# Optimization experiments

Hardware: AMD Instinct MI355X
Metric: run time of the kernel (lower is better)

## Reference

```python
import jax, jax.numpy as jnp
import numpy as np

N_NODES = 100000
N_EDGES = 800000
DIM = 128
BN_EPS = 1e-5


def setup_inputs() -> dict:
    key = jax.random.key(0)
    k1, k2, k3 = jax.random.split(key, 3)
    x = jax.random.normal(k1, (N_NODES, DIM), dtype=jnp.float32)
    edge_index = jax.random.randint(k2, (2, N_EDGES), 0, N_NODES, dtype=jnp.int64)
    # xavier-uniform-like init for the linear weight [out, in]
    limit = float(np.sqrt(6.0 / (DIM + DIM)))
    W = jax.random.uniform(k3, (DIM, DIM), dtype=jnp.float32, minval=-limit, maxval=limit)
    bias = jnp.zeros((DIM,), dtype=jnp.float32)
    bn_gamma = jnp.ones((DIM,), dtype=jnp.float32)
    bn_beta = jnp.zeros((DIM,), dtype=jnp.float32)
    return {"x": x, "edge_index": edge_index, "W": W, "bias": bias,
            "bn_gamma": bn_gamma, "bn_beta": bn_beta, "bit_sum": 0}


def reference(x, edge_index, W, bias, bn_gamma, bn_beta, bit_sum):
    n = x.shape[0]
    # Linear (no bias), is_q=False path; q_xw treated as identity.
    h = x @ W.T                                   # [N, D]
    row, col = edge_index[0], edge_index[1]
    # symmetric degree normalization: deg computed over destination (col)
    deg = jax.ops.segment_sum(jnp.ones_like(col, dtype=h.dtype), col, num_segments=n)
    deg_inv_sqrt = jnp.where(deg > 0, jax.lax.rsqrt(jnp.maximum(deg, 1.0)), 0.0)
    norm = deg_inv_sqrt[row] * deg_inv_sqrt[col]  # [E]
    # message: norm * x_j (x_j = h[row]), aggregate (add) at col
    msg = norm[:, None] * h[row]                  # [E, D]
    out = jax.ops.segment_sum(msg, col, num_segments=n)  # [N, D]
    out = out + bias
    # BatchNorm1d (training mode: batch stats, biased variance)
    mean = jnp.mean(out, axis=0)
    var = jnp.var(out, axis=0)
    out = (out - mean) * jax.lax.rsqrt(var + BN_EPS) * bn_gamma + bn_beta
    # activation
    out = jax.nn.relu(out)
    # residual (in_dim == out_dim); dropout p=0 -> identity
    out = out + x
    return (out, 0)
```

## Files before the change

### kernel.cpp

```cpp
#include <hip/hip_runtime.h>
#include <cstddef>

#define NN 100000
#define DD 128
#define ND (NN * DD)
#define BN_EPS 1e-5f
#define LDA 136
#define NREP 16
#define NBKT 98
#define EPB 4096

typedef __bf16 bf16_t;
typedef bf16_t bf16x8 __attribute__((ext_vector_type(8)));
typedef float f32x4 __attribute__((ext_vector_type(4)));
typedef unsigned int uint;
typedef unsigned short ushort;


__device__ __forceinline__ ushort f2b(float f) {
    uint u = __builtin_bit_cast(uint, f);
    u += 0x7FFFu + ((u >> 16) & 1u);
    return (ushort)(u >> 16);
}
__device__ __forceinline__ float b2f(uint s) {
    return __builtin_bit_cast(float, s << 16);
}

__device__ __forceinline__ int detect_i64(const int* __restrict__ ei) {
    __shared__ int sflag;
    int t = threadIdx.x;
    if (t < 64) {
        int hi = ei[2 * t + 1];
        unsigned long long b = __ballot(hi == 0);
        if (t == 0) sflag = (b == ~0ull) ? 1 : 0;
    }
    __syncthreads();
    return sflag;
}

__global__ __launch_bounds__(256) void k_prep(const int* __restrict__ ei,
                                              int* __restrict__ bktot, int E, int nbh,
                                              const float* __restrict__ x,
                                              uint* __restrict__ xb,
                                              const float* __restrict__ W,
                                              uint* __restrict__ wb) {
    if ((int)blockIdx.x < nbh) {
        int f = detect_i64(ei);
        __shared__ int hist[NBKT];
        int t = threadIdx.x;
        if (t < NBKT) hist[t] = 0;
        __syncthreads();
        int base = blockIdx.x * EPB;
        int count = min(EPB, E - base);
        for (int i = t; i < count; i += 256) {
            int e = base + i;
            int c = f ? ei[2 * (E + e)] : ei[E + e];
            atomicAdd(&hist[c >> 10], 1);
        }
        __syncthreads();
        if (t < NBKT && hist[t] > 0) atomicAdd(&bktot[t], hist[t]);
        return;
    }
    int i = (blockIdx.x - nbh) * 256 + threadIdx.x;
    const float* src;
    uint* dst;
    int j;
    if (i < ND / 8) { src = x; dst = xb; j = i; }
    else { j = i - ND / 8; if (j >= (DD * DD) / 8) return; src = W; dst = wb; }
    const float4* s4 = (const float4*)src;
    float4 a = s4[2 * j], b = s4[2 * j + 1];
    uint4 o;
    o.x = (uint)f2b(a.x) | ((uint)f2b(a.y) << 16);
    o.y = (uint)f2b(a.z) | ((uint)f2b(a.w) << 16);
    o.z = (uint)f2b(b.x) | ((uint)f2b(b.y) << 16);
    o.w = (uint)f2b(b.z) | ((uint)f2b(b.w) << 16);
    ((uint4*)dst)[j] = o;
}

__global__ __launch_bounds__(256) void k_bin(const int* __restrict__ ei,
                                             const int* __restrict__ bktot,
                                             int* __restrict__ bcur,
                                             uint2* __restrict__ pairs, int E) {
    int f = detect_i64(ei);
    __shared__ int bb[NBKT], hist[NBKT], scur[NBKT];
    int t = threadIdx.x;
    if (t < NBKT) { bb[t] = bktot[t]; hist[t] = 0; }
    __syncthreads();
    if (t == 0) {
        int run = 0;
        for (int i = 0; i < NBKT; ++i) { int v = bb[i]; bb[i] = run; run += v; }
    }
    int base = blockIdx.x * EPB;
    int count = min(EPB, E - base);
    int rr[16], cc[16];
#pragma unroll
    for (int k = 0; k < 16; ++k) {
        int i = t + k * 256;
        if (i < count) {
            int e = base + i;
            int r, c;
            if (f) { r = ei[2 * e]; c = ei[2 * (E + e)]; }
            else   { r = ei[e];     c = ei[E + e]; }
            rr[k] = r; cc[k] = c;
            atomicAdd(&hist[c >> 10], 1);
        }
    }
    __syncthreads();
    if (t < NBKT) scur[t] = bb[t] + atomicAdd(&bcur[t], hist[t]);
    __syncthreads();
#pragma unroll
    for (int k = 0; k < 16; ++k) {
        int i = t + k * 256;
        if (i < count) {
            int b = cc[k] >> 10;
            int pos = atomicAdd(&scur[b], 1);
            pairs[pos] = (uint2){(uint)rr[k], (uint)cc[k]};
        }
    }
}

__global__ __launch_bounds__(256) void k_cnt(const uint2* __restrict__ pairs,
                                             const int* __restrict__ bktot,
                                             int* __restrict__ ptr0,
                                             int* __restrict__ cnt,
                                             float* __restrict__ dinv,
                                             int* __restrict__ srow) {
    __shared__ int hist[1024];
    __shared__ int scur[1024];
    __shared__ int ls[256];
    __shared__ int bb[NBKT];
    __shared__ int se0, se1;
    int b = blockIdx.x;
    int t = threadIdx.x;
    if (t < NBKT) bb[t] = bktot[t];
#pragma unroll
    for (int i = 0; i < 4; ++i) hist[t + i * 256] = 0;
    __syncthreads();
    if (t == 0) {
        int run = 0;
        for (int i = 0; i < b; ++i) run += bb[i];
        se0 = run; se1 = run + bb[b];
    }
    __syncthreads();
    int e0 = se0, e1 = se1;
    int nodebase = b << 10;
    for (int i = e0 + t; i < e1; i += 256)
        atomicAdd(&hist[(int)pairs[i].y - nodebase], 1);
    __syncthreads();
    int c4[4];
    int lsum = 0;
#pragma unroll
    for (int i = 0; i < 4; ++i) { c4[i] = hist[t * 4 + i]; lsum += c4[i]; }
    ls[t] = lsum;
    __syncthreads();
    for (int o = 1; o < 256; o <<= 1) {
        int v = (t >= o) ? ls[t - o] : 0;
        __syncthreads();
        ls[t] += v;
        __syncthreads();
    }
    int run = ls[t] - lsum + e0;
#pragma unroll
    for (int i = 0; i < 4; ++i) {
        int idx = nodebase + t * 4 + i;
        if (idx < NN) {
            ptr0[idx] = run;
            cnt[idx] = c4[i];
            dinv[idx] = c4[i] > 0 ? rsqrtf((float)c4[i]) : 0.f;
        }
        scur[t * 4 + i] = run;
        run += c4[i];
    }
    __syncthreads();
    for (int i = e0 + t; i < e1; i += 256) {
        uint2 p = pairs[i];
        int pos = atomicAdd(&scur[(int)p.y - nodebase], 1);
        srow[pos] = (int)p.x;
    }
}

__global__ __launch_bounds__(256, 4) void k_gg(const uint* __restrict__ xb,
                                               const int* __restrict__ srow,
                                               const int* __restrict__ ptr0,
                                               const int* __restrict__ cnt,
                                               const float* __restrict__ dinv,
                                               const ushort* __restrict__ wb,
                                               ushort* __restrict__ hb,
                                               float* __restrict__ csr,
                                               float* __restrict__ cqr) {
    __shared__ char smem[64 * LDA * 2];
    ushort* sAp = (ushort*)smem;
    int t = threadIdx.x;
    int wave = t >> 6, lane = t & 63;
    size_t rowbase = (size_t)blockIdx.x * 64;

    int mn = (int)rowbase + wave * 16 + (lane & 15);
    int sv = 0, kv = 0;
    float dv = 0.f;
    if (lane < 16 && mn < NN) { sv = ptr0[mn]; kv = cnt[mn]; dv = dinv[mn]; }

    for (int i = 0; i < 16; i += 2) {
        int sa0 = __shfl(sv, i),     kA = __shfl(kv, i);
        int sb0 = __shfl(sv, i + 1), kB = __shfl(kv, i + 1);
        float dA = __shfl(dv, i), dB = __shfl(dv, i + 1);
        float axA = 0.f, ayA = 0.f, axB = 0.f, ayB = 0.f;
        int kmax = max(kA, kB);
        for (int base = 0; base < kmax; base += 64) {
            int mA = kA - base; mA = mA > 64 ? 64 : mA;
            int mB = kB - base; mB = mB > 64 ? 64 : mB;
            int rjA = 0, rjB = 0;
            if (lane < mA) rjA = srow[sa0 + base + lane];
            if (lane < mB) rjB = srow[sb0 + base + lane];
            int mm = max(mA, mB);
            for (int j = 0; j < mm; j += 4) {
                int ra0 = __shfl(rjA, j),     rb0 = __shfl(rjB, j);
                int ra1 = __shfl(rjA, j + 1), rb1 = __shfl(rjB, j + 1);
                int ra2 = __shfl(rjA, j + 2), rb2 = __shfl(rjB, j + 2);
                int ra3 = __shfl(rjA, j + 3), rb3 = __shfl(rjB, j + 3);
                uint va0 = xb[(size_t)ra0 * 64 + lane];
                uint vb0 = xb[(size_t)rb0 * 64 + lane];
                uint va1 = xb[(size_t)ra1 * 64 + lane];
                uint vb1 = xb[(size_t)rb1 * 64 + lane];
                uint va2 = xb[(size_t)ra2 * 64 + lane];
                uint vb2 = xb[(size_t)rb2 * 64 + lane];
                uint va3 = xb[(size_t)ra3 * 64 + lane];
                uint vb3 = xb[(size_t)rb3 * 64 + lane];
                float wa0 = dinv[ra0], wbb0 = dinv[rb0];
                float wa1 = dinv[ra1], wbb1 = dinv[rb1];
                float wa2 = dinv[ra2], wbb2 = dinv[rb2];
                float wa3 = dinv[ra3], wbb3 = dinv[rb3];
                wa0 = (j     < mA) ? wa0 : 0.f;  wbb0 = (j     < mB) ? wbb0 : 0.f;
                wa1 = (j + 1 < mA) ? wa1 : 0.f;  wbb1 = (j + 1 < mB) ? wbb1 : 0.f;
                wa2 = (j + 2 < mA) ? wa2 : 0.f;  wbb2 = (j + 2 < mB) ? wbb2 : 0.f;
                wa3 = (j + 3 < mA) ? wa3 : 0.f;  wbb3 = (j + 3 < mB) ? wbb3 : 0.f;
                axA = fmaf(wa0, b2f(va0 & 0xFFFFu), axA); ayA = fmaf(wa0, b2f(va0 >> 16), ayA);
                axA = fmaf(wa1, b2f(va1 & 0xFFFFu), axA); ayA = fmaf(wa1, b2f(va1 >> 16), ayA);
                axA = fmaf(wa2, b2f(va2 & 0xFFFFu), axA); ayA = fmaf(wa2, b2f(va2 >> 16), ayA);
                axA = fmaf(wa3, b2f(va3 & 0xFFFFu), axA); ayA = fmaf(wa3, b2f(va3 >> 16), ayA);
                axB = fmaf(wbb0, b2f(vb0 & 0xFFFFu), axB); ayB = fmaf(wbb0, b2f(vb0 >> 16), ayB);
                axB = fmaf(wbb1, b2f(vb1 & 0xFFFFu), axB); ayB = fmaf(wbb1, b2f(vb1 >> 16), ayB);
                axB = fmaf(wbb2, b2f(vb2 & 0xFFFFu), axB); ayB = fmaf(wbb2, b2f(vb2 >> 16), ayB);
                axB = fmaf(wbb3, b2f(vb3 & 0xFFFFu), axB); ayB = fmaf(wbb3, b2f(vb3 >> 16), ayB);
            }
        }
        *(uint*)(sAp + (wave * 16 + i) * LDA + lane * 2) =
            (uint)f2b(dA * axA) | ((uint)f2b(dA * ayA) << 16);
        *(uint*)(sAp + (wave * 16 + i + 1) * LDA + lane * 2) =
            (uint)f2b(dB * axB) | ((uint)f2b(dB * ayB) << 16);
    }
    __syncthreads();

    int quad = lane >> 4, l16 = lane & 15;
    bf16x8 Af[4];
#pragma unroll
    for (int ks = 0; ks < 4; ++ks)
        Af[ks] = __builtin_bit_cast(
            bf16x8, *(const uint4*)(sAp + (wave * 16 + l16) * LDA + ks * 32 + quad * 8));
    __syncthreads();
    float (*cp)[128] = (float (*)[128])smem;
    float (*cq)[128] = (float (*)[128])(smem + 4 * 128 * 4);

#pragma unroll
    for (int ct = 0; ct < 8; ++ct) {
        bf16x8 Bf[4];
#pragma unroll
        for (int ks = 0; ks < 4; ++ks)
            Bf[ks] = __builtin_bit_cast(
                bf16x8,
                *(const uint4*)(wb + (size_t)(ct * 16 + l16) * 128 + ks * 32 + quad * 8));
        f32x4 acc = (f32x4){0.f, 0.f, 0.f, 0.f};
#pragma unroll
        for (int ks = 0; ks < 4; ++ks)
            acc = __builtin_amdgcn_mfma_f32_16x16x32_bf16(Af[ks], Bf[ks], acc, 0, 0, 0);
        float ss = 0.f, qq = 0.f;
#pragma unroll
        for (int r = 0; r < 4; ++r) {
            float v = acc[r];
            ss += v; qq += v * v;
            size_t row = rowbase + wave * 16 + quad * 4 + r;
            if (row < NN) hb[row * 128 + ct * 16 + l16] = f2b(v);
        }
        ss += __shfl_xor(ss, 16); ss += __shfl_xor(ss, 32);
        qq += __shfl_xor(qq, 16); qq += __shfl_xor(qq, 32);
        if (quad == 0) { cp[wave][ct * 16 + l16] = ss; cq[wave][ct * 16 + l16] = qq; }
    }
    __syncthreads();
    if (t < 128) {
        int rep = (blockIdx.x & (NREP - 1)) * 128 + t;
        atomicAdd(&csr[rep], cp[0][t] + cp[1][t] + cp[2][t] + cp[3][t]);
        atomicAdd(&cqr[rep], cq[0][t] + cq[1][t] + cq[2][t] + cq[3][t]);
    }
}

__global__ __launch_bounds__(256) void k_final(const uint* __restrict__ hb,
                                               const uint* __restrict__ xb,
                                               const float* __restrict__ gamma,
                                               const float* __restrict__ beta,
                                               const float* __restrict__ csr,
                                               const float* __restrict__ cqr,
                                               float* __restrict__ out, int out_size) {
    __shared__ float sa[128], sb[128];
    int t = threadIdx.x;
    const float invN = 1.0f / NN;
    if (t < 128) {
        float s = 0.f;
        for (int i = 0; i < NREP; ++i) s += csr[i * 128 + t];
        sa[t] = s * invN;
    } else {
        int c = t - 128;
        float s = 0.f;
        for (int i = 0; i < NREP; ++i) s += cqr[i * 128 + c];
        sb[c] = s * invN;
    }
    __syncthreads();
    if (t < 128) {
        float m = sa[t];
        float var = sb[t] - m * m;
        float inv = rsqrtf(var + BN_EPS);
        float A = inv * gamma[t];
        float B = beta[t] - m * A;
        sa[t] = A; sb[t] = B;
    }
    __syncthreads();

    int c0 = (t & 7) * 16;
    int u8 = blockIdx.x * 512 + t * 2;
    uint4 hv0 = ((const uint4*)hb)[u8], hv1 = ((const uint4*)hb)[u8 + 1];
    uint4 xv0 = ((const uint4*)xb)[u8], xv1 = ((const uint4*)xb)[u8 + 1];
    uint hu[8] = {hv0.x, hv0.y, hv0.z, hv0.w, hv1.x, hv1.y, hv1.z, hv1.w};
    uint xu[8] = {xv0.x, xv0.y, xv0.z, xv0.w, xv1.x, xv1.y, xv1.z, xv1.w};
    float res[16];
#pragma unroll
    for (int p = 0; p < 8; ++p) {
        int c = c0 + p * 2;
        float h0 = b2f(hu[p] & 0xFFFFu), h1 = b2f(hu[p] >> 16);
        float x0 = b2f(xu[p] & 0xFFFFu), x1 = b2f(xu[p] >> 16);
        res[2 * p]     = fmaxf(fmaf(h0, sa[c],     sb[c]),     0.f) + x0;
        res[2 * p + 1] = fmaxf(fmaf(h1, sa[c + 1], sb[c + 1]), 0.f) + x1;
    }
    float4* o4 = (float4*)out;
    int ob = blockIdx.x * 1024 + t * 4;
#pragma unroll
    for (int q = 0; q < 4; ++q)
        o4[ob + q] = (float4){res[4 * q], res[4 * q + 1], res[4 * q + 2], res[4 * q + 3]};
    if (blockIdx.x == 0 && t == 0 && out_size > ND) out[ND] = 0.0f;
}

extern "C" void kernel_launch(void* const* d_in, const int* in_sizes, int n_in,
                              void* d_out, int out_size, void* d_ws, size_t ws_size,
                              hipStream_t stream) {
    const float* x     = (const float*)d_in[0];
    const int*   ei    = (const int*)d_in[1];
    const float* W     = (const float*)d_in[2];
    const float* gamma = (const float*)d_in[4];
    const float* beta  = (const float*)d_in[5];
    float* ws = (float*)d_ws;
    float* out = (float*)d_out;

    uint*   hb       = (uint*)ws;
    uint*   xb       = hb + ND / 2;
    float*  csr      = (float*)(xb + ND / 2);
    float*  cqr      = csr + NREP * 128;
    int*    bktot    = (int*)(cqr + NREP * 128);
    int*    bcur     = bktot + 128;
    int*    cnt      = bcur + 128;
    int*    ptr0     = cnt + NN;
    float*  dinv     = (float*)(ptr0 + NN);
    int*    srow     = (int*)(dinv + NN);

    int E = in_sizes[1] / 2;
    uint* wb = (uint*)(srow + E);

    uint2* pairs = (uint2*)hb;

    int nbc = (ND / 8 + (DD * DD) / 8 + 255) / 256;
    int nbin = (E + EPB - 1) / EPB;

    hipMemsetAsync(csr, 0, (size_t)(2 * NREP * 128 + 256) * 4, stream);
    k_prep<<<nbin + nbc, 256, 0, stream>>>(ei, bktot, E, nbin, x, xb, W, wb);
    k_bin<<<nbin, 256, 0, stream>>>(ei, bktot, bcur, pairs, E);
    k_cnt<<<NBKT, 256, 0, stream>>>(pairs, bktot, ptr0, cnt, dinv, srow);
    k_gg<<<(NN + 63) / 64, 256, 0, stream>>>(xb, srow, ptr0, cnt, dinv,
                                             (const ushort*)wb, (ushort*)hb, csr, cqr);
    k_final<<<ND / 4096, 256, 0, stream>>>(hb, xb, gamma, beta, csr, cqr,
                                           out, out_size);
}
```

Before: 231.2 us.

## Double waves per block in gather-GEMM kernel and split MFMA columns across waves

The gather+GEMM kernel now runs 512 threads per block, so each wave gathers 8 destination rows instead of 16. After the sync, 4 row groups by 2 column halves split the MFMA work, and per-wave partial sums are reduced for the BN statistics. Halving the serial gather per wave aims to add memory-level parallelism and shorten the per-block critical path. Index math also moves from 64-bit to 32-bit to cut address arithmetic. The launch bound of 8 blocks of 512 threads per CU may push register pressure higher.

Result: no change. 227.7 us (-1.5%).

```diff
diff --git a/kernel.cpp b/kernel.cpp
--- a/kernel.cpp
+++ b/kernel.cpp
@@ -179,7 +179,7 @@
     }
 }
 
-__global__ __launch_bounds__(256, 4) void k_gg(const uint* __restrict__ xb,
+__global__ __launch_bounds__(512, 8) void k_gg(const uint* __restrict__ xb,
                                                const int* __restrict__ srow,
                                                const int* __restrict__ ptr0,
                                                const int* __restrict__ cnt,
@@ -192,14 +192,14 @@
     ushort* sAp = (ushort*)smem;
     int t = threadIdx.x;
     int wave = t >> 6, lane = t & 63;
-    size_t rowbase = (size_t)blockIdx.x * 64;
-
-    int mn = (int)rowbase + wave * 16 + (lane & 15);
+    uint rowbase = (uint)blockIdx.x * 64;
+
+    int mn = (int)rowbase + wave * 8 + (lane & 7);
     int sv = 0, kv = 0;
     float dv = 0.f;
-    if (lane < 16 && mn < NN) { sv = ptr0[mn]; kv = cnt[mn]; dv = dinv[mn]; }
-
-    for (int i = 0; i < 16; i += 2) {
+    if (lane < 8 && mn < NN) { sv = ptr0[mn]; kv = cnt[mn]; dv = dinv[mn]; }
+
+    for (int i = 0; i < 8; i += 2) {
         int sa0 = __shfl(sv, i),     kA = __shfl(kv, i);
         int sb0 = __shfl(sv, i + 1), kB = __shfl(kv, i + 1);
         float dA = __shfl(dv, i), dB = __shfl(dv, i + 1);
@@ -217,14 +217,14 @@
                 int ra1 = __shfl(rjA, j + 1), rb1 = __shfl(rjB, j + 1);
                 int ra2 = __shfl(rjA, j + 2), rb2 = __shfl(rjB, j + 2);
                 int ra3 = __shfl(rjA, j + 3), rb3 = __shfl(rjB, j + 3);
-                uint va0 = xb[(size_t)ra0 * 64 + lane];
-                uint vb0 = xb[(size_t)rb0 * 64 + lane];
-                uint va1 = xb[(size_t)ra1 * 64 + lane];
-                uint vb1 = xb[(size_t)rb1 * 64 + lane];
-                uint va2 = xb[(size_t)ra2 * 64 + lane];
-                uint vb2 = xb[(size_t)rb2 * 64 + lane];
-                uint va3 = xb[(size_t)ra3 * 64 + lane];
-                uint vb3 = xb[(size_t)rb3 * 64 + lane];
+                uint va0 = xb[((uint)ra0 << 6) + (uint)lane];
+                uint vb0 = xb[((uint)rb0 << 6) + (uint)lane];
+                uint va1 = xb[((uint)ra1 << 6) + (uint)lane];
+                uint vb1 = xb[((uint)rb1 << 6) + (uint)lane];
+                uint va2 = xb[((uint)ra2 << 6) + (uint)lane];
+                uint vb2 = xb[((uint)rb2 << 6) + (uint)lane];
+                uint va3 = xb[((uint)ra3 << 6) + (uint)lane];
+                uint vb3 = xb[((uint)rb3 << 6) + (uint)lane];
                 float wa0 = dinv[ra0], wbb0 = dinv[rb0];
                 float wa1 = dinv[ra1], wbb1 = dinv[rb1];
                 float wa2 = dinv[ra2], wbb2 = dinv[rb2];
@@ -243,31 +243,33 @@
                 axB = fmaf(wbb3, b2f(vb3 & 0xFFFFu), axB); ayB = fmaf(wbb3, b2f(vb3 >> 16), ayB);
             }
         }
-        *(uint*)(sAp + (wave * 16 + i) * LDA + lane * 2) =
+        *(uint*)(sAp + (wave * 8 + i) * LDA + lane * 2) =
             (uint)f2b(dA * axA) | ((uint)f2b(dA * ayA) << 16);
-        *(uint*)(sAp + (wave * 16 + i + 1) * LDA + lane * 2) =
+        *(uint*)(sAp + (wave * 8 + i + 1) * LDA + lane * 2) =
             (uint)f2b(dB * axB) | ((uint)f2b(dB * ayB) << 16);
     }
     __syncthreads();
 
+    int rg = wave & 3, chh = wave >> 2;
     int quad = lane >> 4, l16 = lane & 15;
     bf16x8 Af[4];
 #pragma unroll
     for (int ks = 0; ks < 4; ++ks)
         Af[ks] = __builtin_bit_cast(
-            bf16x8, *(const uint4*)(sAp + (wave * 16 + l16) * LDA + ks * 32 + quad * 8));
-    __syncthreads();
-    float (*cp)[128] = (float (*)[128])smem;
-    float (*cq)[128] = (float (*)[128])(smem + 4 * 128 * 4);
-
-#pragma unroll
-    for (int ct = 0; ct < 8; ++ct) {
+            bf16x8, *(const uint4*)(sAp + (rg * 16 + l16) * LDA + ks * 32 + quad * 8));
+    __syncthreads();
+    float (*cp)[64] = (float (*)[64])smem;
+    float (*cq)[64] = (float (*)[64])(smem + 8 * 64 * 4);
+
+#pragma unroll
+    for (int c = 0; c < 4; ++c) {
+        int ctg = chh * 4 + c;
         bf16x8 Bf[4];
 #pragma unroll
         for (int ks = 0; ks < 4; ++ks)
             Bf[ks] = __builtin_bit_cast(
                 bf16x8,
-                *(const uint4*)(wb + (size_t)(ct * 16 + l16) * 128 + ks * 32 + quad * 8));
+                *(const uint4*)(wb + (uint)(ctg * 16 + l16) * 128 + ks * 32 + quad * 8));
         f32x4 acc = (f32x4){0.f, 0.f, 0.f, 0.f};
 #pragma unroll
         for (int ks = 0; ks < 4; ++ks)
@@ -277,18 +279,21 @@
         for (int r = 0; r < 4; ++r) {
             float v = acc[r];
             ss += v; qq += v * v;
-            size_t row = rowbase + wave * 16 + quad * 4 + r;
-            if (row < NN) hb[row * 128 + ct * 16 + l16] = f2b(v);
+            uint row = rowbase + rg * 16 + quad * 4 + r;
+            if (row < NN) hb[row * 128u + (uint)(ctg * 16 + l16)] = f2b(v);
         }
         ss += __shfl_xor(ss, 16); ss += __shfl_xor(ss, 32);
         qq += __shfl_xor(qq, 16); qq += __shfl_xor(qq, 32);
-        if (quad == 0) { cp[wave][ct * 16 + l16] = ss; cq[wave][ct * 16 + l16] = qq; }
+        if (quad == 0) { cp[wave][c * 16 + l16] = ss; cq[wave][c * 16 + l16] = qq; }
     }
     __syncthreads();
     if (t < 128) {
+        int w0 = (t >> 6) * 4, lc = t & 63;
+        float s = cp[w0][lc] + cp[w0 + 1][lc] + cp[w0 + 2][lc] + cp[w0 + 3][lc];
+        float q = cq[w0][lc] + cq[w0 + 1][lc] + cq[w0 + 2][lc] + cq[w0 + 3][lc];
         int rep = (blockIdx.x & (NREP - 1)) * 128 + t;
-        atomicAdd(&csr[rep], cp[0][t] + cp[1][t] + cp[2][t] + cp[3][t]);
-        atomicAdd(&cqr[rep], cq[0][t] + cq[1][t] + cq[2][t] + cq[3][t]);
+        atomicAdd(&csr[rep], s);
+        atomicAdd(&cqr[rep], q);
     }
 }
 
@@ -380,7 +385,7 @@
     k_prep<<<nbin + nbc, 256, 0, stream>>>(ei, bktot, E, nbin, x, xb, W, wb);
     k_bin<<<nbin, 256, 0, stream>>>(ei, bktot, bcur, pairs, E);
     k_cnt<<<NBKT, 256, 0, stream>>>(pairs, bktot, ptr0, cnt, dinv, srow);
-    k_gg<<<(NN + 63) / 64, 256, 0, stream>>>(xb, srow, ptr0, cnt, dinv,
+    k_gg<<<(NN + 63) / 64, 512, 0, stream>>>(xb, srow, ptr0, cnt, dinv,
                                              (const ushort*)wb, (ushort*)hb, csr, cqr);
     k_final<<<ND / 4096, 256, 0, stream>>>(hb, xb, gamma, beta, csr, cqr,
                                            out, out_size);
```
